# Kernel tuning notes

Hardware: AMD Instinct MI355X
Metric: run time of the kernel (lower is better)

## Reference

```python
import jax, jax.numpy as jnp
import numpy as np

N_NODES = 50000
N_EDGES = 400000
B = 2
NUM_STEP = 2
# SAGEConv layer dims (in, out): conv1..conv6
LAYER_DIMS = [(64, 128), (128, 64), (64, 32), (32, 32), (64, 64), (128, 64)]


def setup_inputs() -> dict:
    key = jax.random.key(0)
    ks = jax.random.split(key, 4 + 3 * len(LAYER_DIMS))
    inp = {
        "in_feat": jax.random.normal(ks[0], (B, N_NODES, 64), dtype=jnp.float32),
        "src": jax.random.randint(ks[1], (N_EDGES,), 0, N_NODES, dtype=jnp.int32),
        "dst": jax.random.randint(ks[2], (N_EDGES,), 0, N_NODES, dtype=jnp.int32),
    }
    for i, (fin, fout) in enumerate(LAYER_DIMS, start=1):
        scale = jnp.float32(1.0 / np.sqrt(fin))
        inp[f"w_self{i}"] = jax.random.normal(ks[3 * i], (fin, fout), dtype=jnp.float32) * scale
        inp[f"w_neigh{i}"] = jax.random.normal(ks[3 * i + 1], (fin, fout), dtype=jnp.float32) * scale
        inp[f"b{i}"] = jnp.zeros((fout,), dtype=jnp.float32)
    return inp


def reference(in_feat, src, dst,
              w_self1, w_neigh1, b1, w_self2, w_neigh2, b2,
              w_self3, w_neigh3, b3, w_self4, w_neigh4, b4,
              w_self5, w_neigh5, b5, w_self6, w_neigh6, b6):
    # in_feat: [B, N, F] -> internal [N, B, F] (matches torch transpose(0,1))
    h = jnp.transpose(in_feat, (1, 0, 2))
    # in-degree per dst node for mean aggregation (0-degree nodes -> agg 0)
    deg = jax.ops.segment_sum(jnp.ones(src.shape[0], jnp.float32), dst,
                              num_segments=N_NODES)
    deg = jnp.maximum(deg, 1.0)[:, None, None]  # [N,1,1]

    def sage(x, ws, wn, b):
        # DGL SAGEConv (mean): fc_self(h) + fc_neigh(mean_{u in N(v)} h_u) + b
        agg = jax.ops.segment_sum(x[src], dst, num_segments=N_NODES) / deg
        return x @ ws + agg @ wn + b

    for _ in range(NUM_STEP):
        h1 = jax.nn.relu(sage(h, w_self1, w_neigh1, b1))
        h2 = jax.nn.relu(sage(h1, w_self2, w_neigh2, b2))
        h3 = jax.nn.relu(sage(h2, w_self3, w_neigh3, b3))
        h4 = jnp.concatenate(
            [jax.nn.relu(sage(h3, w_self4, w_neigh4, b4)), h3], axis=2)
        h5 = jnp.concatenate(
            [jax.nn.relu(sage(h4, w_self5, w_neigh5, b5)), h4], axis=2)
        h = sage(h5, w_self6, w_neigh6, b6)
    return jnp.transpose(h, (1, 0, 2))
```

## Files before the change

### kernel.cpp

```cpp
#include <hip/hip_runtime.h>

#define NN 50000
#define NE 400000
#define BB 2
#define ROWS (NN * BB)

#define SCAN_CHUNK 1024
#define SCAN_NB ((NN + SCAN_CHUNK - 1) / SCAN_CHUNK)

__device__ inline void fma4(float4& a, float s, const float4& w) {
    a.x = fmaf(s, w.x, a.x); a.y = fmaf(s, w.y, a.y);
    a.z = fmaf(s, w.z, a.z); a.w = fmaf(s, w.w, a.w);
}
__device__ inline void add4(float4& a, const float4& v) {
    a.x += v.x; a.y += v.y; a.z += v.z; a.w += v.w;
}


__global__ void k_hist(const int* __restrict__ dst, int* __restrict__ deg) {
    int e = blockIdx.x * 256 + threadIdx.x;
    if (e < NE) atomicAdd(&deg[dst[e]], 1);
}

__global__ __launch_bounds__(256) void k_scan1(const int* __restrict__ deg,
                                               int* __restrict__ bsum) {
    int b = blockIdx.x, t = threadIdx.x;
    int base = b * SCAN_CHUNK + t * 4;
    int s = 0;
#pragma unroll
    for (int i = 0; i < 4; i++) {
        int idx = base + i;
        if (idx < NN) s += deg[idx];
    }
    for (int d = 32; d; d >>= 1) s += __shfl_down(s, d);
    __shared__ int ws[4];
    if ((t & 63) == 0) ws[t >> 6] = s;
    __syncthreads();
    if (t == 0) bsum[b] = ws[0] + ws[1] + ws[2] + ws[3];
}

__global__ void k_scan2(const int* __restrict__ bsum, int* __restrict__ boff,
                        int* __restrict__ rowoff_last) {
    int lane = threadIdx.x;
    int v = (lane < SCAN_NB) ? bsum[lane] : 0;
    int incl = v;
    for (int d = 1; d < 64; d <<= 1) {
        int o = __shfl_up(incl, d);
        if (lane >= d) incl += o;
    }
    if (lane < SCAN_NB) boff[lane] = incl - v;
    if (lane == 63) rowoff_last[0] = incl;
}

__global__ __launch_bounds__(256) void k_scan3(const int* __restrict__ deg,
                                               const int* __restrict__ boff,
                                               int* __restrict__ rowoff,
                                               int* __restrict__ cursor,
                                               float* __restrict__ rdeg) {
    int b = blockIdx.x, t = threadIdx.x;
    int lane = t & 63, wv = t >> 6;
    int base = b * SCAN_CHUNK + t * 4;
    int dv[4];
    int ts = 0;
#pragma unroll
    for (int i = 0; i < 4; i++) {
        int idx = base + i;
        dv[i] = (idx < NN) ? deg[idx] : 0;
        ts += dv[i];
    }
    int incl = ts;
    for (int d = 1; d < 64; d <<= 1) {
        int o = __shfl_up(incl, d);
        if (lane >= d) incl += o;
    }
    __shared__ int wsum[4];
    if (lane == 63) wsum[wv] = incl;
    __syncthreads();
    int wexc = 0;
    for (int w = 0; w < wv; w++) wexc += wsum[w];
    int run = boff[b] + wexc + (incl - ts);
#pragma unroll
    for (int i = 0; i < 4; i++) {
        int idx = base + i;
        if (idx < NN) {
            rowoff[idx] = run;
            cursor[idx] = run;
            rdeg[idx] = 1.0f / fmaxf((float)dv[i], 1.0f);
            run += dv[i];
        }
    }
}

__global__ void k_fill(const int* __restrict__ src, const int* __restrict__ dst,
                       int* __restrict__ cursor, int* __restrict__ csr) {
    int e = blockIdx.x * 256 + threadIdx.x;
    if (e >= NE) return;
    int pos = atomicAdd(&cursor[dst[e]], 1);
    csr[pos] = src[e];
}


__global__ void k_tin(const float4* __restrict__ in, float4* __restrict__ out) {
    int t = blockIdx.x * 256 + threadIdx.x;
    if (t >= ROWS * 16) return;
    int r = t >> 4, c = t & 15;
    int n = r >> 1, b = r & 1;
    out[t] = in[(b * NN + n) * 16 + c];
}

__global__ void k_gather(const float4* __restrict__ x, const int* __restrict__ csr,
                         const int* __restrict__ rowoff, const float* __restrict__ rdeg,
                         float4* __restrict__ out, int w4s,
                         int xp4, int xo4, int op4, int oo4) {
    int t = blockIdx.x * 256 + threadIdx.x;
    int n = t >> w4s, tid = t & ((1 << w4s) - 1);
    if (n >= NN) return;
    int beg = rowoff[n], end = rowoff[n + 1];
    int a0 = xo4 + tid;
    int xp2 = 2 * xp4;
    float4 c00 = {0.f,0.f,0.f,0.f}, c01 = {0.f,0.f,0.f,0.f};
    float4 c10 = {0.f,0.f,0.f,0.f}, c11 = {0.f,0.f,0.f,0.f};
    int j = beg;
    for (; j + 4 <= end; j += 4) {
        int s0 = csr[j], s1 = csr[j+1], s2 = csr[j+2], s3 = csr[j+3];
        int b0 = s0 * xp2 + a0, b1 = s1 * xp2 + a0;
        int b2 = s2 * xp2 + a0, b3 = s3 * xp2 + a0;
        float4 p0 = x[b0], q0 = x[b0 + xp4];
        float4 p1 = x[b1], q1 = x[b1 + xp4];
        float4 p2 = x[b2], q2 = x[b2 + xp4];
        float4 p3 = x[b3], q3 = x[b3 + xp4];
        add4(c00, p0); add4(c10, q0); add4(c01, p1); add4(c11, q1);
        add4(c00, p2); add4(c10, q2); add4(c01, p3); add4(c11, q3);
    }
    for (; j < end; j++) {
        int s = csr[j];
        int b = s * xp2 + a0;
        add4(c00, x[b]); add4(c10, x[b + xp4]);
    }
    float rd = rdeg[n];
    float4 o0 = {(c00.x+c01.x)*rd, (c00.y+c01.y)*rd, (c00.z+c01.z)*rd, (c00.w+c01.w)*rd};
    float4 o1 = {(c10.x+c11.x)*rd, (c10.y+c11.y)*rd, (c10.z+c11.z)*rd, (c10.w+c11.w)*rd};
    out[(2*n)     * op4 + oo4 + tid] = o0;
    out[(2*n + 1) * op4 + oo4 + tid] = o1;
}

template<int FIN, int FOUT, int MODE, bool RELU, bool TRANS, int RPT, int NCQ>
__global__ __launch_bounds__(256) void k_gemm(
    const float* __restrict__ x, const float* __restrict__ agg,
    const float* __restrict__ w0, const float* __restrict__ w1,
    const float* __restrict__ bias, float* __restrict__ out,
    int xpitch4, int xoff4, int apitch4, int aoff4, int ostride4, int ooff4)
{
    constexpr int NQ = FOUT / 4;
    constexpr int TX = NQ / NCQ;
    constexpr int TY = 256 / TX;
    constexpr int TM = TY * RPT;
    constexpr int W4 = FIN * FOUT / 4;
    constexpr int NW = (MODE == 1) ? 2 : 1;

    __shared__ float4 wlds[NW * W4];

    int t = threadIdx.x;
    const float4* w0v = (const float4*)w0;
    for (int i = t; i < W4; i += 256) wlds[i] = w0v[i];
    if (MODE == 1) {
        const float4* w1v = (const float4*)w1;
        for (int i = t; i < W4; i += 256) wlds[W4 + i] = w1v[i];
    }
    __syncthreads();

    int tx = t % TX, ty = t / TX;
    int rbase = blockIdx.x * TM + ty * RPT;

    int xb[RPT], ab[RPT];
#pragma unroll
    for (int i = 0; i < RPT; i++) {
        int r = rbase + i;
        r = r < ROWS ? r : ROWS - 1;
        xb[i] = r * xpitch4 + xoff4;
        ab[i] = r * apitch4 + aoff4;
    }

    float4 acc[RPT][NCQ];
#pragma unroll
    for (int i = 0; i < RPT; i++)
#pragma unroll
        for (int j = 0; j < NCQ; j++) acc[i][j] = make_float4(0.f, 0.f, 0.f, 0.f);

    const float4* xv4 = (const float4*)x;
    const float4* av4 = (const float4*)agg;

    for (int k4 = 0; k4 < FIN / 4; k4++) {
        float4 wq[4][NCQ], nq[4][NCQ];
#pragma unroll
        for (int u = 0; u < 4; u++)
#pragma unroll
            for (int j = 0; j < NCQ; j++) {
                wq[u][j] = wlds[(k4 * 4 + u) * NQ + tx + j * TX];
                if (MODE == 1) nq[u][j] = wlds[W4 + (k4 * 4 + u) * NQ + tx + j * TX];
            }
#pragma unroll
        for (int i = 0; i < RPT; i++) {
            float4 xv = xv4[xb[i] + k4];
#pragma unroll
            for (int j = 0; j < NCQ; j++) {
                fma4(acc[i][j], xv.x, wq[0][j]); fma4(acc[i][j], xv.y, wq[1][j]);
                fma4(acc[i][j], xv.z, wq[2][j]); fma4(acc[i][j], xv.w, wq[3][j]);
            }
            if (MODE == 1) {
                float4 av = av4[ab[i] + k4];
#pragma unroll
                for (int j = 0; j < NCQ; j++) {
                    fma4(acc[i][j], av.x, nq[0][j]); fma4(acc[i][j], av.y, nq[1][j]);
                    fma4(acc[i][j], av.z, nq[2][j]); fma4(acc[i][j], av.w, nq[3][j]);
                }
            }
        }
    }

    float4 b4[NCQ];
#pragma unroll
    for (int j = 0; j < NCQ; j++) {
        b4[j] = make_float4(0.f, 0.f, 0.f, 0.f);
        if (MODE != 0) b4[j] = *(const float4*)&bias[(tx + j * TX) * 4];
    }

#pragma unroll
    for (int i = 0; i < RPT; i++) {
        int r = rbase + i;
        if (r >= ROWS) continue;
#pragma unroll
        for (int j = 0; j < NCQ; j++) {
            int q = tx + j * TX;
            float4 v = acc[i][j];
            if (MODE == 2) {
                float4 ag = av4[ab[i] + q];
                add4(v, ag);
            }
            if (MODE != 0) add4(v, b4[j]);
            if (RELU) {
                v.x = fmaxf(v.x, 0.f); v.y = fmaxf(v.y, 0.f);
                v.z = fmaxf(v.z, 0.f); v.w = fmaxf(v.w, 0.f);
            }
            int oidx;
            if (TRANS) {
                int n = r >> 1, b = r & 1;
                oidx = b * (NN * 16) + n * 16 + q;
            } else {
                oidx = r * ostride4 + ooff4 + q;
            }
            ((float4*)out)[oidx] = v;
        }
    }
}


template<int FIN, int FOUT, int MODE, bool RELU, bool TRANS, int RPT = 8, int NCQ = 1>
static void launch_gemm(const float* x, const float* agg, const float* w0, const float* w1,
                        const float* bias, float* out, int xpitch4, int xoff4,
                        int apitch4, int aoff4, int ostride4, int ooff4,
                        hipStream_t stream) {
    constexpr int TM = (256 / (FOUT / 4 / NCQ)) * RPT;
    int nb = (ROWS + TM - 1) / TM;
    k_gemm<FIN, FOUT, MODE, RELU, TRANS, RPT, NCQ><<<nb, 256, 0, stream>>>(
        x, agg, w0, w1, bias, out, xpitch4, xoff4, apitch4, aoff4, ostride4, ooff4);
}

static void launch_gather(const float* x, const int* csr, const int* rowoff,
                          const float* rdeg, float* aggb, int width,
                          int xpitch4, int xoff4, int opitch4, int ooff4,
                          hipStream_t stream) {
    int w4s = 0;
    while ((1 << w4s) < width / 4) w4s++;
    int gt = NN << w4s;
    k_gather<<<(gt + 255) / 256, 256, 0, stream>>>(
        (const float4*)x, csr, rowoff, rdeg, (float4*)aggb, w4s,
        xpitch4, xoff4, opitch4, ooff4);
}

extern "C" void kernel_launch(void* const* d_in, const int* in_sizes, int n_in,
                              void* d_out, int out_size, void* d_ws, size_t ws_size,
                              hipStream_t stream) {
    const float* in_feat = (const float*)d_in[0];
    const int* src = (const int*)d_in[1];
    const int* dst = (const int*)d_in[2];
    const float* Ws[6], *Wn[6], *Bi[6];
    for (int i = 0; i < 6; i++) {
        Ws[i] = (const float*)d_in[3 + 3 * i];
        Wn[i] = (const float*)d_in[4 + 3 * i];
        Bi[i] = (const float*)d_in[5 + 3 * i];
    }

    char* ws = (char*)d_ws;
    size_t off = 0;
    auto alloc = [&](size_t bytes) {
        void* p = ws + off;
        off = (off + bytes + 255) & ~(size_t)255;
        return p;
    };
    float* rdeg   = (float*)alloc((size_t)NN * 4);
    int*   deg    = (int*)  alloc((size_t)NN * 4);
    int*   rowoff = (int*)  alloc((size_t)(NN + 1) * 4);
    int*   cursor = (int*)  alloc((size_t)NN * 4);
    int*   csr    = (int*)  alloc((size_t)NE * 4);
    int*   bsum   = (int*)  alloc((size_t)SCAN_NB * 4);
    int*   boff   = (int*)  alloc((size_t)SCAN_NB * 4);
    float* bufH   = (float*)alloc((size_t)ROWS * 64 * 4);
    float* bufA   = (float*)alloc((size_t)ROWS * 128 * 4);
    float* bufB   = (float*)alloc((size_t)ROWS * 128 * 4);
    float* aggb   = (float*)alloc((size_t)ROWS * 64 * 4);
    float* zbuf   = (float*)d_out;

    hipMemsetAsync(deg, 0, (size_t)NN * 4, stream);
    k_hist<<<(NE + 255) / 256, 256, 0, stream>>>(dst, deg);
    k_scan1<<<SCAN_NB, 256, 0, stream>>>(deg, bsum);
    k_scan2<<<1, 64, 0, stream>>>(bsum, boff, rowoff + NN);
    k_scan3<<<SCAN_NB, 256, 0, stream>>>(deg, boff, rowoff, cursor, rdeg);
    k_fill<<<(NE + 255) / 256, 256, 0, stream>>>(src, dst, cursor, csr);

    k_tin<<<(ROWS * 16 + 255) / 256, 256, 0, stream>>>((const float4*)in_feat, (float4*)bufH);

    for (int s = 0; s < 2; s++) {
        int last = (s == 1);

        launch_gather(bufH, csr, rowoff, rdeg, aggb, 64, 16, 0, 16, 0, stream);
        launch_gemm<64, 128, 1, true, false, 8, 2>(bufH, aggb, Ws[0], Wn[0], Bi[0],
                                                   bufA, 16, 0, 16, 0, 32, 0, stream);

        launch_gemm<128, 64, 0, false, false, 8, 2>(bufA, nullptr, Wn[1], nullptr, nullptr,
                                                    zbuf, 32, 0, 0, 0, 16, 0, stream);
        launch_gather(zbuf, csr, rowoff, rdeg, aggb, 64, 16, 0, 16, 0, stream);
        launch_gemm<128, 64, 2, true, false, 8, 2>(bufA, aggb, Ws[1], nullptr, Bi[1],
                                                   bufH, 32, 0, 16, 0, 16, 0, stream);

        launch_gemm<64, 32, 0, false, false, 8, 1>(bufH, nullptr, Wn[2], nullptr, nullptr,
                                                   zbuf, 16, 0, 0, 0, 8, 0, stream);
        launch_gather(zbuf, csr, rowoff, rdeg, aggb, 32, 8, 0, 8, 0, stream);
        launch_gemm<64, 32, 2, true, false, 8, 1>(bufH, aggb, Ws[2], nullptr, Bi[2],
                                                  bufB, 16, 0, 8, 0, 32, 24, stream);

        launch_gather(bufB, csr, rowoff, rdeg, aggb, 32, 32, 24, 16, 8, stream);
        launch_gemm<32, 32, 1, true, false, 8, 1>(bufB, aggb, Ws[3], Wn[3], Bi[3],
                                                  bufB, 32, 24, 16, 8, 32, 16, stream);

        launch_gather(bufB, csr, rowoff, rdeg, aggb, 32, 32, 16, 16, 0, stream);
        launch_gemm<64, 64, 1, true, false, 8, 2>(bufB, aggb, Ws[4], Wn[4], Bi[4],
                                                  bufB, 32, 16, 16, 0, 32, 0, stream);

        launch_gemm<128, 64, 0, false, false, 8, 2>(bufB, nullptr, Wn[5], nullptr, nullptr,
                                                    zbuf, 32, 0, 0, 0, 16, 0, stream);
        launch_gather(zbuf, csr, rowoff, rdeg, aggb, 64, 16, 0, 16, 0, stream);
        if (last) {
            launch_gemm<128, 64, 2, false, true, 8, 2>(bufB, aggb, Ws[5], nullptr, Bi[5],
                                                       (float*)d_out, 32, 0, 16, 0, 16, 0, stream);
        } else {
            launch_gemm<128, 64, 2, false, false, 8, 2>(bufB, aggb, Ws[5], nullptr, Bi[5],
                                                        bufH, 32, 0, 16, 0, 16, 0, stream);
        }
    }
}
```

Baseline: 1.116 ms.

## Store projected neighbor features in bf16 and read input directly

```diff
diff --git a/kernel.cpp b/kernel.cpp
--- a/kernel.cpp
+++ b/kernel.cpp
@@ -14,6 +14,17 @@
 }
 __device__ inline void add4(float4& a, const float4& v) {
     a.x += v.x; a.y += v.y; a.z += v.z; a.w += v.w;
+}
+__device__ inline unsigned bf2(float a, float b) {
+    unsigned ua = __float_as_uint(a); ua = (ua + 0x7FFFu + ((ua >> 16) & 1u)) >> 16;
+    unsigned ub = __float_as_uint(b); ub = (ub + 0x7FFFu + ((ub >> 16) & 1u)) >> 16;
+    return ua | (ub << 16);
+}
+__device__ inline void bfadd(float4& lo, float4& hi, uint4 v) {
+    lo.x += __uint_as_float(v.x << 16); lo.y += __uint_as_float(v.x & 0xFFFF0000u);
+    lo.z += __uint_as_float(v.y << 16); lo.w += __uint_as_float(v.y & 0xFFFF0000u);
+    hi.x += __uint_as_float(v.z << 16); hi.y += __uint_as_float(v.z & 0xFFFF0000u);
+    hi.z += __uint_as_float(v.w << 16); hi.w += __uint_as_float(v.w & 0xFFFF0000u);
 }
 
 
@@ -100,42 +111,33 @@
 }
 
 
-__global__ void k_tin(const float4* __restrict__ in, float4* __restrict__ out) {
-    int t = blockIdx.x * 256 + threadIdx.x;
-    if (t >= ROWS * 16) return;
-    int r = t >> 4, c = t & 15;
-    int n = r >> 1, b = r & 1;
-    out[t] = in[(b * NN + n) * 16 + c];
-}
-
 __global__ void k_gather(const float4* __restrict__ x, const int* __restrict__ csr,
                          const int* __restrict__ rowoff, const float* __restrict__ rdeg,
                          float4* __restrict__ out, int w4s,
-                         int xp4, int xo4, int op4, int oo4) {
+                         int xns4, int xbs4, int xo4, int op4, int oo4) {
     int t = blockIdx.x * 256 + threadIdx.x;
     int n = t >> w4s, tid = t & ((1 << w4s) - 1);
     if (n >= NN) return;
     int beg = rowoff[n], end = rowoff[n + 1];
     int a0 = xo4 + tid;
-    int xp2 = 2 * xp4;
     float4 c00 = {0.f,0.f,0.f,0.f}, c01 = {0.f,0.f,0.f,0.f};
     float4 c10 = {0.f,0.f,0.f,0.f}, c11 = {0.f,0.f,0.f,0.f};
     int j = beg;
     for (; j + 4 <= end; j += 4) {
         int s0 = csr[j], s1 = csr[j+1], s2 = csr[j+2], s3 = csr[j+3];
-        int b0 = s0 * xp2 + a0, b1 = s1 * xp2 + a0;
-        int b2 = s2 * xp2 + a0, b3 = s3 * xp2 + a0;
-        float4 p0 = x[b0], q0 = x[b0 + xp4];
-        float4 p1 = x[b1], q1 = x[b1 + xp4];
-        float4 p2 = x[b2], q2 = x[b2 + xp4];
-        float4 p3 = x[b3], q3 = x[b3 + xp4];
+        int b0 = s0 * xns4 + a0, b1 = s1 * xns4 + a0;
+        int b2 = s2 * xns4 + a0, b3 = s3 * xns4 + a0;
+        float4 p0 = x[b0], q0 = x[b0 + xbs4];
+        float4 p1 = x[b1], q1 = x[b1 + xbs4];
+        float4 p2 = x[b2], q2 = x[b2 + xbs4];
+        float4 p3 = x[b3], q3 = x[b3 + xbs4];
         add4(c00, p0); add4(c10, q0); add4(c01, p1); add4(c11, q1);
         add4(c00, p2); add4(c10, q2); add4(c01, p3); add4(c11, q3);
     }
     for (; j < end; j++) {
         int s = csr[j];
-        int b = s * xp2 + a0;
-        add4(c00, x[b]); add4(c10, x[b + xp4]);
+        int b = s * xns4 + a0;
+        add4(c00, x[b]); add4(c10, x[b + xbs4]);
     }
     float rd = rdeg[n];
     float4 o0 = {(c00.x+c01.x)*rd, (c00.y+c01.y)*rd, (c00.z+c01.z)*rd, (c00.w+c01.w)*rd};
@@ -144,28 +146,67 @@
     out[(2*n + 1) * op4 + oo4 + tid] = o1;
 }
 
-template<int FIN, int FOUT, int MODE, bool RELU, bool TRANS, int RPT, int NCQ>
+__global__ void k_gather_bf(const uint4* __restrict__ x, const int* __restrict__ csr,
+                            const int* __restrict__ rowoff, const float* __restrict__ rdeg,
+                            float4* __restrict__ out, int w8s, int op4, int oo4) {
+    int t = blockIdx.x * 256 + threadIdx.x;
+    int n = t >> w8s, tid = t & ((1 << w8s) - 1);
+    if (n >= NN) return;
+    int rp8 = 1 << w8s, nrp = 2 << w8s;
+    int beg = rowoff[n], end = rowoff[n + 1];
+    float4 a0l = {0.f,0.f,0.f,0.f}, a0h = {0.f,0.f,0.f,0.f};
+    float4 a1l = {0.f,0.f,0.f,0.f}, a1h = {0.f,0.f,0.f,0.f};
+    int j = beg;
+    for (; j + 2 <= end; j += 2) {
+        int s0 = csr[j], s1 = csr[j+1];
+        int b0 = s0 * nrp + tid, b1 = s1 * nrp + tid;
+        uint4 p0 = x[b0], q0 = x[b0 + rp8];
+        uint4 p1 = x[b1], q1 = x[b1 + rp8];
+        bfadd(a0l, a0h, p0); bfadd(a1l, a1h, q0);
+        bfadd(a0l, a0h, p1); bfadd(a1l, a1h, q1);
+    }
+    if (j < end) {
+        int s = csr[j];
+        int b = s * nrp + tid;
+        bfadd(a0l, a0h, x[b]); bfadd(a1l, a1h, x[b + rp8]);
+    }
+    float rd = rdeg[n];
+    float4 o0l = {a0l.x*rd, a0l.y*rd, a0l.z*rd, a0l.w*rd};
+    float4 o0h = {a0h.x*rd, a0h.y*rd, a0h.z*rd, a0h.w*rd};
+    float4 o1l = {a1l.x*rd, a1l.y*rd, a1l.z*rd, a1l.w*rd};
+    float4 o1h = {a1h.x*rd, a1h.y*rd, a1h.z*rd, a1h.w*rd};
+    int r0 = (2*n) * op4 + oo4 + 2*tid;
+    int r1 = (2*n + 1) * op4 + oo4 + 2*tid;
+    out[r0] = o0l; out[r0 + 1] = o0h;
+    out[r1] = o1l; out[r1 + 1] = o1h;
+}
+
+template<int FIN, int FOUT, int MODE, bool RELU, bool TRANS, int RPT, int NCQ, int CS, bool OBF>
 __global__ __launch_bounds__(256) void k_gemm(
     const float* __restrict__ x, const float* __restrict__ agg,
     const float* __restrict__ w0, const float* __restrict__ w1,
     const float* __restrict__ bias, float* __restrict__ out,
-    int xpitch4, int xoff4, int apitch4, int aoff4, int ostride4, int ooff4)
+    int xns4, int xbs4, int xo4, int apitch4, int aoff4, int ostride4, int ooff4)
 {
     constexpr int NQ = FOUT / 4;
-    constexpr int TX = NQ / NCQ;
+    constexpr int NQB = NQ / CS;
+    constexpr int TX = NQB / NCQ;
     constexpr int TY = 256 / TX;
     constexpr int TM = TY * RPT;
-    constexpr int W4 = FIN * FOUT / 4;
+    constexpr int W4B = FIN * NQB;
     constexpr int NW = (MODE == 1) ? 2 : 1;
 
-    __shared__ float4 wlds[NW * W4];
+    __shared__ float4 wlds[NW * W4B];
 
     int t = threadIdx.x;
+    int cq0 = blockIdx.y * NQB;
     const float4* w0v = (const float4*)w0;
-    for (int i = t; i < W4; i += 256) wlds[i] = w0v[i];
+    for (int i = t; i < W4B; i += 256)
+        wlds[i] = w0v[(i / NQB) * NQ + cq0 + (i % NQB)];
     if (MODE == 1) {
         const float4* w1v = (const float4*)w1;
-        for (int i = t; i < W4; i += 256) wlds[W4 + i] = w1v[i];
+        for (int i = t; i < W4B; i += 256)
+            wlds[W4B + i] = w1v[(i / NQB) * NQ + cq0 + (i % NQB)];
     }
     __syncthreads();
 
@@ -177,7 +218,7 @@
     for (int i = 0; i < RPT; i++) {
         int r = rbase + i;
         r = r < ROWS ? r : ROWS - 1;
-        xb[i] = r * xpitch4 + xoff4;
+        xb[i] = (r >> 1) * xns4 + (r & 1) * xbs4 + xo4;
         ab[i] = r * apitch4 + aoff4;
     }
 
@@ -196,8 +237,8 @@
         for (int u = 0; u < 4; u++)
 #pragma unroll
             for (int j = 0; j < NCQ; j++) {
-                wq[u][j] = wlds[(k4 * 4 + u) * NQ + tx + j * TX];
-                if (MODE == 1) nq[u][j] = wlds[W4 + (k4 * 4 + u) * NQ + tx + j * TX];
+                wq[u][j] = wlds[(k4 * 4 + u) * NQB + tx + j * TX];
+                if (MODE == 1) nq[u][j] = wlds[W4B + (k4 * 4 + u) * NQB + tx + j * TX];
             }
 #pragma unroll
         for (int i = 0; i < RPT; i++) {
@@ -222,7 +263,7 @@
 #pragma unroll
     for (int j = 0; j < NCQ; j++) {
         b4[j] = make_float4(0.f, 0.f, 0.f, 0.f);
-        if (MODE != 0) b4[j] = *(const float4*)&bias[(tx + j * TX) * 4];
+        if (MODE != 0) b4[j] = *(const float4*)&bias[(cq0 + tx + j * TX) * 4];
     }
 
 #pragma unroll
@@ -231,7 +272,7 @@
         if (r >= ROWS) continue;
 #pragma unroll
         for (int j = 0; j < NCQ; j++) {
-            int q = tx + j * TX;
+            int q = cq0 + tx + j * TX;
             float4 v = acc[i][j];
             if (MODE == 2) {
                 float4 ag = av4[ab[i] + q];
@@ -242,40 +283,57 @@
                 v.x = fmaxf(v.x, 0.f); v.y = fmaxf(v.y, 0.f);
                 v.z = fmaxf(v.z, 0.f); v.w = fmaxf(v.w, 0.f);
             }
-            int oidx;
-            if (TRANS) {
-                int n = r >> 1, b = r & 1;
-                oidx = b * (NN * 16) + n * 16 + q;
+            if (OBF) {
+                uint2 w; w.x = bf2(v.x, v.y); w.y = bf2(v.z, v.w);
+                ((uint2*)out)[r * ostride4 + ooff4 + q] = w;
             } else {
-                oidx = r * ostride4 + ooff4 + q;
-            }
-            ((float4*)out)[oidx] = v;
+                int oidx;
+                if (TRANS) {
+                    int n = r >> 1, b = r & 1;
+                    oidx = b * (NN * 16) + n * 16 + q;
+                } else {
+                    oidx = r * ostride4 + ooff4 + q;
+                }
+                ((float4*)out)[oidx] = v;
+            }
         }
     }
 }
 
 
-template<int FIN, int FOUT, int MODE, bool RELU, bool TRANS, int RPT = 8, int NCQ = 1>
+template<int FIN, int FOUT, int MODE, bool RELU, bool TRANS,
+         int RPT = 8, int NCQ = 1, int CS = 1, bool OBF = false>
 static void launch_gemm(const float* x, const float* agg, const float* w0, const float* w1,
-                        const float* bias, float* out, int xpitch4, int xoff4,
+                        const float* bias, float* out, int xns4, int xbs4, int xo4,
                         int apitch4, int aoff4, int ostride4, int ooff4,
                         hipStream_t stream) {
-    constexpr int TM = (256 / (FOUT / 4 / NCQ)) * RPT;
+    constexpr int TM = (256 / (FOUT / 4 / CS / NCQ)) * RPT;
     int nb = (ROWS + TM - 1) / TM;
-    k_gemm<FIN, FOUT, MODE, RELU, TRANS, RPT, NCQ><<<nb, 256, 0, stream>>>(
-        x, agg, w0, w1, bias, out, xpitch4, xoff4, apitch4, aoff4, ostride4, ooff4);
+    k_gemm<FIN, FOUT, MODE, RELU, TRANS, RPT, NCQ, CS, OBF>
+        <<<dim3(nb, CS), 256, 0, stream>>>(
+        x, agg, w0, w1, bias, out, xns4, xbs4, xo4, apitch4, aoff4, ostride4, ooff4);
 }
 
 static void launch_gather(const float* x, const int* csr, const int* rowoff,
                           const float* rdeg, float* aggb, int width,
-                          int xpitch4, int xoff4, int opitch4, int ooff4,
+                          int xns4, int xbs4, int xo4, int op4, int oo4,
                           hipStream_t stream) {
     int w4s = 0;
     while ((1 << w4s) < width / 4) w4s++;
     int gt = NN << w4s;
     k_gather<<<(gt + 255) / 256, 256, 0, stream>>>(
         (const float4*)x, csr, rowoff, rdeg, (float4*)aggb, w4s,
-        xpitch4, xoff4, opitch4, ooff4);
+        xns4, xbs4, xo4, op4, oo4);
+}
+
+static void launch_gather_bf(const float* z, const int* csr, const int* rowoff,
+                             const float* rdeg, float* aggb, int width,
+                             int op4, int oo4, hipStream_t stream) {
+    int w8s = 0;
+    while ((1 << w8s) < width / 8) w8s++;
+    int gt = NN << w8s;
+    k_gather_bf<<<(gt + 255) / 256, 256, 0, stream>>>(
+        (const uint4*)z, csr, rowoff, rdeg, (float4*)aggb, w8s, op4, oo4);
 }
 
 extern "C" void kernel_launch(void* const* d_in, const int* in_sizes, int n_in,
@@ -318,44 +376,46 @@
     k_scan3<<<SCAN_NB, 256, 0, stream>>>(deg, boff, rowoff, cursor, rdeg);
     k_fill<<<(NE + 255) / 256, 256, 0, stream>>>(src, dst, cursor, csr);
 
-    k_tin<<<(ROWS * 16 + 255) / 256, 256, 0, stream>>>((const float4*)in_feat, (float4*)bufH);
+    const int BSTR = NN * 16;
 
     for (int s = 0; s < 2; s++) {
         int last = (s == 1);
-
-        launch_gather(bufH, csr, rowoff, rdeg, aggb, 64, 16, 0, 16, 0, stream);
-        launch_gemm<64, 128, 1, true, false, 8, 2>(bufH, aggb, Ws[0], Wn[0], Bi[0],
-                                                   bufA, 16, 0, 16, 0, 32, 0, stream);
-
-        launch_gemm<128, 64, 0, false, false, 8, 2>(bufA, nullptr, Wn[1], nullptr, nullptr,
-                                                    zbuf, 32, 0, 0, 0, 16, 0, stream);
-        launch_gather(zbuf, csr, rowoff, rdeg, aggb, 64, 16, 0, 16, 0, stream);
+        const float* hx = s ? bufH : in_feat;
+        int hns = s ? 32 : 16, hbs = s ? 16 : BSTR;
+
+        launch_gather(hx, csr, rowoff, rdeg, aggb, 64, hns, hbs, 0, 16, 0, stream);
+        launch_gemm<64, 128, 1, true, false, 8, 2, 2>(hx, aggb, Ws[0], Wn[0], Bi[0],
+                                                      bufA, hns, hbs, 0, 16, 0, 32, 0, stream);
+
+        launch_gemm<128, 64, 0, false, false, 8, 2, 1, true>(
+            bufA, nullptr, Wn[1], nullptr, nullptr, zbuf, 64, 32, 0, 0, 0, 16, 0, stream);
+        launch_gather_bf(zbuf, csr, rowoff, rdeg, aggb, 64, 16, 0, stream);
         launch_gemm<128, 64, 2, true, false, 8, 2>(bufA, aggb, Ws[1], nullptr, Bi[1],
-                                                   bufH, 32, 0, 16, 0, 16, 0, stream);
-
-        launch_gemm<64, 32, 0, false, false, 8, 1>(bufH, nullptr, Wn[2], nullptr, nullptr,
-                                                   zbuf, 16, 0, 0, 0, 8, 0, stream);
-        launch_gather(zbuf, csr, rowoff, rdeg, aggb, 32, 8, 0, 8, 0, stream);
+                                                   bufH, 64, 32, 0, 16, 0, 16, 0, stream);
+
+        launch_gemm<64, 32, 0, false, false, 8, 1, 1, true>(
+            bufH, nullptr, Wn[2], nullptr, nullptr, zbuf, 32, 16, 0, 0, 0, 8, 0, stream);
+        launch_gather_bf(zbuf, csr, rowoff, rdeg, aggb, 32, 8, 0, stream);
         launch_gemm<64, 32, 2, true, false, 8, 1>(bufH, aggb, Ws[2], nullptr, Bi[2],
-                                                  bufB, 16, 0, 8, 0, 32, 24, stream);
-
-        launch_gather(bufB, csr, rowoff, rdeg, aggb, 32, 32, 24, 16, 8, stream);
+                                                  bufB, 32, 16, 0, 8, 0, 32, 24, stream);
+
+        launch_gather(bufB, csr, rowoff, rdeg, aggb, 32, 64, 32, 24, 16, 8, stream);
         launch_gemm<32, 32, 1, true, false, 8, 1>(bufB, aggb, Ws[3], Wn[3], Bi[3],
-                                                  bufB, 32, 24, 16, 8, 32, 16, stream);
-
-        launch_gather(bufB, csr, rowoff, rdeg, aggb, 32, 32, 16, 16, 0, stream);
+                                                  bufB, 64, 32, 24, 16, 8, 32, 16, stream);
+
+        launch_gather(bufB, csr, rowoff, rdeg, aggb, 32, 64, 32, 16, 16, 0, stream);
         launch_gemm<64, 64, 1, true, false, 8, 2>(bufB, aggb, Ws[4], Wn[4], Bi[4],
-                                                  bufB, 32, 16, 16, 0, 32, 0, stream);
-
-        launch_gemm<128, 64, 0, false, false, 8, 2>(bufB, nullptr, Wn[5], nullptr, nullptr,
-                                                    zbuf, 32, 0, 0, 0, 16, 0, stream);
-        launch_gather(zbuf, csr, rowoff, rdeg, aggb, 64, 16, 0, 16, 0, stream);
+                                                  bufB, 64, 32, 16, 16, 0, 32, 0, stream);
+
+        launch_gemm<128, 64, 0, false, false, 8, 2, 1, true>(
+            bufB, nullptr, Wn[5], nullptr, nullptr, zbuf, 64, 32, 0, 0, 0, 16, 0, stream);
+        launch_gather_bf(zbuf, csr, rowoff, rdeg, aggb, 64, 16, 0, stream);
         if (last) {
             launch_gemm<128, 64, 2, false, true, 8, 2>(bufB, aggb, Ws[5], nullptr, Bi[5],
-                                                       (float*)d_out, 32, 0, 16, 0, 16, 0, stream);
+                                                       (float*)d_out, 64, 32, 0, 16, 0, 16, 0, stream);
         } else {
             launch_gemm<128, 64, 2, false, false, 8, 2>(bufB, aggb, Ws[5], nullptr, Bi[5],
-                                                        bufH, 32, 0, 16, 0, 16, 0, stream);
+                                                        bufH, 64, 32, 0, 16, 0, 16, 0, stream);
         }
     }
 }
```

New measurement: 1.108 ms. No clear change (-0.7%).
